# Kernel tuning notes

Hardware: AMD Instinct MI355X
Metric: run time of the kernel (lower is better)

## Reference

```python
import jax, jax.numpy as jnp
import numpy as np

N_TV_ITER = 20      # fixed Chambolle iteration count (skimage early-stops via eps; fixed for jit)
TV_WEIGHT = 0.1


def _div(p):
    # negative adjoint of forward-difference gradient (skimage convention)
    d = -(p[0] + p[1])
    d = d.at[1:, :].add(p[0, :-1, :])
    d = d.at[:, 1:].add(p[1, :, :-1])
    return d


def tv_chambolle_2d(image):
    """skimage.restoration.denoise_tv_chambolle on a single 2D image, weight=0.1."""
    tau = 0.25  # 1 / (2 * ndim)

    def step(p, _):
        out = image + _div(p)
        gy = jnp.zeros_like(out).at[:-1, :].set(out[1:, :] - out[:-1, :])
        gx = jnp.zeros_like(out).at[:, :-1].set(out[:, 1:] - out[:, :-1])
        norm = jnp.sqrt(gy * gy + gx * gx)
        g = jnp.stack([gy, gx])
        p = (p - tau * g) / (1.0 + (tau / TV_WEIGHT) * norm)
        return p, None

    p0 = jnp.zeros((2,) + image.shape, image.dtype)
    p, _ = jax.lax.scan(step, p0, None, length=N_TV_ITER)
    return image + _div(p)


def tv_denoise(img):  # [B,C,H,W], vmapped over B*C (replaces the CPU python loop)
    B, C, H, W = img.shape
    out = jax.vmap(tv_chambolle_2d)(img.reshape(B * C, H, W))
    return out.reshape(B, C, H, W)


def conv(x, w, stride=1, groups=1):
    pad = w.shape[2] // 2  # 'same'-style padding for odd kernels, 0 for 1x1
    return jax.lax.conv_general_dilated(
        x, w, (stride, stride), [(pad, pad), (pad, pad)],
        dimension_numbers=('NCHW', 'OIHW', 'NCHW'),
        feature_group_count=groups)


def haar_ll(x):
    # one level of pywt wavedec2('haar') LL band: 0.5 * sum over each 2x2 block
    return 0.5 * (x[..., ::2, ::2] + x[..., ::2, 1::2] + x[..., 1::2, ::2] + x[..., 1::2, 1::2])


def backbone(x, stem_w, dw_pw):
    # stride-32, 1280-channel EfficientNet-B0-style feature extractor
    x = jax.nn.silu(conv(x, stem_w, stride=2))
    for dw, pw in dw_pw:
        x = jax.nn.silu(conv(x, dw, stride=2, groups=dw.shape[0]))
        x = jax.nn.silu(conv(x, pw))
    return x


def setup_inputs() -> dict:
    key = jax.random.key(0)
    ks = jax.random.split(key, 16)
    B, H, W = 4, 512, 512

    def w(k, o, i, kh, kw):
        return jax.random.normal(k, (o, i, kh, kw), jnp.float32) * (1.0 / np.sqrt(i * kh * kw))

    return {
        "img": jax.random.normal(ks[0], (B, 1, H, W), jnp.float32),
        "stem_w": w(ks[1], 32, 1, 3, 3),
        "dw1_w": w(ks[2], 32, 1, 3, 3),  "pw1_w": w(ks[3], 64, 32, 1, 1),
        "dw2_w": w(ks[4], 64, 1, 3, 3),  "pw2_w": w(ks[5], 128, 64, 1, 1),
        "dw3_w": w(ks[6], 128, 1, 3, 3), "pw3_w": w(ks[7], 256, 128, 1, 1),
        "dw4_w": w(ks[8], 256, 1, 3, 3), "pw4_w": w(ks[9], 512, 256, 1, 1),
        "head_w": w(ks[10], 1280, 512, 1, 1),
        "proj_w": w(ks[11], 64, 1280, 1, 1),
        "proj_b": jnp.zeros((64,), jnp.float32),
        "final_w": w(ks[12], 1, 64, 1, 1),
        "final_b": jnp.zeros((1,), jnp.float32),
    }


def reference(img, stem_w, dw1_w, pw1_w, dw2_w, pw2_w, dw3_w, pw3_w, dw4_w, pw4_w,
              head_w, proj_w, proj_b, final_w, final_b):
    B, C, H, W = img.shape
    x = tv_denoise(img)                                     # fused TV Chambolle
    x = backbone(x, stem_w, [(dw1_w, pw1_w), (dw2_w, pw2_w), (dw3_w, pw3_w), (dw4_w, pw4_w)])
    x = jax.nn.silu(conv(x, head_w))                        # [B,1280,H/32,W/32]
    x = conv(x, proj_w) + proj_b[None, :, None, None]       # [B,64,H/32,W/32]
    x = jax.image.resize(x, (B, 64, H, W), method='bilinear')  # align_corners=False semantics
    ll = haar_ll(haar_ll(x))                                # 2-level Haar LL: [B,64,H/4,W/4]
    out = conv(ll, final_w) + final_b[None, :, None, None]  # [B,1,H/4,W/4]
    return out
```

## Files before the change

### kernel.cpp

```cpp
#include <hip/hip_runtime.h>
#include <math.h>

constexpr int BATCH = 4;
constexpr int IMG_H = 512, IMG_W = 512;
constexpr int IMG_HW = IMG_H * IMG_W;
constexpr int PSTR = BATCH * IMG_HW;

constexpr size_t O_PA   = 0;
constexpr size_t O_PB   = O_PA + 2 * (size_t)PSTR;
constexpr size_t O_DEN  = O_PB + 2 * (size_t)PSTR;
constexpr size_t O_A1   = O_DEN + (size_t)PSTR;
constexpr size_t O_A2   = O_A1 + 8388608;
constexpr size_t O_WT1  = O_A2 + 2097152;
constexpr size_t O_WT2  = O_WT1 + 32 * 64;
constexpr size_t O_WT3  = O_WT2 + 64 * 128;
constexpr size_t O_WT4  = O_WT3 + 128 * 256;
constexpr size_t O_WTH  = O_WT4 + 256 * 512;
constexpr size_t O_WCOMB= O_WTH + 512 * 1280;
constexpr size_t O_BCOMB= O_WCOMB + 1280;
constexpr size_t O_S    = O_BCOMB + 4;
constexpr size_t WS_FLOATS = O_S + 1024;

__device__ __forceinline__ float fast_rcp(float x) { return __builtin_amdgcn_rcpf(x); }
__device__ __forceinline__ float fast_sqrt(float x) { return __builtin_amdgcn_sqrtf(x); }
__device__ __forceinline__ float silu_f(float x) {
    float e = __builtin_amdgcn_exp2f(-1.44269504088896f * x);
    return x * fast_rcp(1.0f + e);
}
__device__ __forceinline__ int clampi(int v, int lo, int hi) {
    return v < lo ? lo : (v > hi ? hi : v);
}

template <int NST, bool FIRST, bool LAST>
__global__ __launch_bounds__(512, 8) void tv_reg(const float* __restrict__ img,
                                                 const float* __restrict__ pin,
                                                 float* __restrict__ pout,
                                                 const float* __restrict__ pw1,
                                                 const float* __restrict__ pw2,
                                                 const float* __restrict__ pw3,
                                                 const float* __restrict__ pw4,
                                                 const float* __restrict__ headw,
                                                 const float* __restrict__ projw,
                                                 const float* __restrict__ projb,
                                                 const float* __restrict__ finalw,
                                                 float* __restrict__ ws) {
    constexpr int ROWS = 6, NW = 8, HL = 10, TC = 44, TR = 28;
    constexpr int TVY = 19;
    __shared__ float bndP[2][512], bndO[2][512];

    if constexpr (FIRST) {
        if (blockIdx.y >= TVY) {
            __shared__ float tt[32][33];
            const int tid = threadIdx.x;
            const int pid = ((blockIdx.y - TVY) * 4 + blockIdx.z) * 12 + blockIdx.x;
            for (int t = pid; t < 814; t += 96) {
                const float* src = nullptr; float* dst = nullptr;
                int C = 0, R = 0, tr = 0, tc = 0;
                if (t < 640) {
                    src = headw; dst = ws + O_WTH; R = 1280; C = 512; tr = t >> 4; tc = t & 15;
                } else if (t < 768) {
                    int e = t - 640; src = pw4; dst = ws + O_WT4; R = 512; C = 256; tr = e >> 3; tc = e & 7;
                } else if (t < 800) {
                    int e = t - 768; src = pw3; dst = ws + O_WT3; R = 256; C = 128; tr = e >> 2; tc = e & 3;
                } else if (t < 808) {
                    int e = t - 800; src = pw2; dst = ws + O_WT2; R = 128; C = 64; tr = e >> 1; tc = e & 1;
                } else if (t < 810) {
                    int e = t - 808; src = pw1; dst = ws + O_WT1; R = 64; C = 32; tr = e; tc = 0;
                }
                const int tx = tid & 31, ty = tid >> 5;
                __syncthreads();
                if (src) {
#pragma unroll
                    for (int j = 0; j < 2; ++j)
                        tt[ty + j * 16][tx] =
                            src[(size_t)(tr * 32 + ty + j * 16) * C + tc * 32 + tx];
                }
                __syncthreads();
                if (src) {
#pragma unroll
                    for (int j = 0; j < 2; ++j)
                        dst[(size_t)(tc * 32 + ty + j * 16) * R + tr * 32 + tx] =
                            tt[tx][ty + j * 16];
                } else if (t < 813) {
                    int k = (t - 810) * 512 + tid;
                    if (k < 1280) {
                        float a = 0.0f;
                        for (int ch = 0; ch < 64; ++ch)
                            a = fmaf(finalw[ch], projw[ch * 1280 + k], a);
                        ws[O_WCOMB + k] = a;
                    }
                } else {
                    if (tid == 0) {
                        float a = 0.0f;
                        for (int ch = 0; ch < 64; ++ch) a = fmaf(finalw[ch], projb[ch], a);
                        ws[O_BCOMB] = a;
                    }
                }
            }
            return;
        }
    }

    const int tid = threadIdx.x;
    const int lane = tid & 63, w = tid >> 6;
    const int b = blockIdx.z;
    const int r0 = blockIdx.y * TR, c0 = blockIdx.x * TC;
    const int gj = c0 - HL + lane;
    const int gjc = clampi(gj, 0, 511);
    const int gib = r0 - HL + w * ROWS;
    const float* I = img + b * IMG_HW;
    const bool interior = (r0 - HL >= 1) && (r0 + NW * ROWS - HL <= 511) &&
                          (c0 - HL >= 1) && (c0 + 64 - HL <= 511);

    float rim[ROWS], rp0[ROWS], rp1[ROWS], ro[ROWS];
#pragma unroll
    for (int k = 0; k < ROWS; ++k) {
        int gi = clampi(gib + k, 0, 511);
        rim[k] = I[(gi << 9) + gjc];
    }
    if (!FIRST) {
        const float* P0 = pin + b * IMG_HW;
        const float* P1 = pin + PSTR + b * IMG_HW;
#pragma unroll
        for (int k = 0; k < ROWS; ++k) {
            int gi = clampi(gib + k, 0, 511);
            rp0[k] = P0[(gi << 9) + gjc];
            rp1[k] = P1[(gi << 9) + gjc];
        }
    }
    const bool gjpos = (gj > 0), gjlt = (gj < 511);

    int s0 = 0;
    if (FIRST) {
        bndO[0][tid] = rim[0];
        __syncthreads();
        float odn = (w < NW - 1) ? bndO[0][tid + 64] : 0.0f;
        if (interior) {
#pragma unroll
            for (int k = 0; k < ROWS; ++k) {
                float oR = __shfl_down(rim[k], 1);
                float od = (k < ROWS - 1) ? rim[k + 1] : odn;
                float gy = od - rim[k];
                float gx = oR - rim[k];
                float inv = fast_rcp(fmaf(2.5f, fast_sqrt(fmaf(gy, gy, gx * gx)), 1.0f));
                rp0[k] = -0.25f * gy * inv;
                rp1[k] = -0.25f * gx * inv;
            }
        } else {
#pragma unroll
            for (int k = 0; k < ROWS; ++k) {
                float oR = __shfl_down(rim[k], 1);
                float od = (k < ROWS - 1) ? rim[k + 1] : odn;
                int gi = gib + k;
                float gy = (gi < 511) ? od - rim[k] : 0.0f;
                float gx = gjlt ? oR - rim[k] : 0.0f;
                float inv = fast_rcp(fmaf(2.5f, fast_sqrt(fmaf(gy, gy, gx * gx)), 1.0f));
                rp0[k] = -0.25f * gy * inv;
                rp1[k] = -0.25f * gx * inv;
            }
        }
        s0 = 1;
    }

    for (int s = s0; s < NST; ++s) {
        const int par = s & 1;
        float p1l0 = __shfl_up(rp1[0], 1);
        float partO = rim[0] - rp0[0] - rp1[0];
        if (interior) partO += p1l0;
        else if (gjpos) partO += p1l0;
        bndP[par][tid] = rp0[ROWS - 1];
        bndO[par][tid] = partO;
        __syncthreads();
        float pup0 = (w > 0) ? bndP[par][tid - 64] : 0.0f;
        float odn = (w < NW - 1) ? bndO[par][tid + 64] + rp0[ROWS - 1] : 0.0f;
        if (interior) {
            ro[0] = partO + pup0;
#pragma unroll
            for (int k = 1; k < ROWS; ++k) {
                float p1l = __shfl_up(rp1[k], 1);
                ro[k] = rim[k] - rp0[k] - rp1[k] + rp0[k - 1] + p1l;
            }
#pragma unroll
            for (int k = 0; k < ROWS; ++k) {
                float oR = __shfl_down(ro[k], 1);
                float od = (k < ROWS - 1) ? ro[k + 1] : odn;
                float gy = od - ro[k];
                float gx = oR - ro[k];
                float inv = fast_rcp(fmaf(2.5f, fast_sqrt(fmaf(gy, gy, gx * gx)), 1.0f));
                rp0[k] = (rp0[k] - 0.25f * gy) * inv;
                rp1[k] = (rp1[k] - 0.25f * gx) * inv;
            }
        } else {
            ro[0] = partO + ((gib > 0) ? pup0 : 0.0f);
#pragma unroll
            for (int k = 1; k < ROWS; ++k) {
                float p1l = __shfl_up(rp1[k], 1);
                float o = rim[k] - rp0[k] - rp1[k];
                if (gib + k > 0) o += rp0[k - 1];
                if (gjpos) o += p1l;
                ro[k] = o;
            }
#pragma unroll
            for (int k = 0; k < ROWS; ++k) {
                float oR = __shfl_down(ro[k], 1);
                float od = (k < ROWS - 1) ? ro[k + 1] : odn;
                int gi = gib + k;
                float gy = (gi < 511) ? od - ro[k] : 0.0f;
                float gx = gjlt ? oR - ro[k] : 0.0f;
                float inv = fast_rcp(fmaf(2.5f, fast_sqrt(fmaf(gy, gy, gx * gx)), 1.0f));
                rp0[k] = (rp0[k] - 0.25f * gy) * inv;
                rp1[k] = (rp1[k] - 0.25f * gx) * inv;
            }
        }
    }

    const bool cst = (lane >= HL && lane < HL + TC && gj < 512);
    if (LAST) {
        constexpr int epar = NST & 1;
        bndP[epar][tid] = rp0[ROWS - 1];
        __syncthreads();
        float pup0 = (w > 0) ? bndP[epar][tid - 64] : 0.0f;
        float* D = pout + b * IMG_HW;
#pragma unroll
        for (int k = 0; k < ROWS; ++k) {
            float p1l = __shfl_up(rp1[k], 1);
            int gi = gib + k;
            int rk = w * ROWS + k;
            float o = rim[k] - rp0[k] - rp1[k];
            float pup = (k > 0) ? rp0[k - 1] : pup0;
            if (gi > 0) o += pup;
            if (gjpos) o += p1l;
            if (rk >= HL && rk < HL + TR && cst && gi < 512) D[(gi << 9) + gj] = o;
        }
    } else {
        float* Q0 = pout + b * IMG_HW;
        float* Q1 = pout + PSTR + b * IMG_HW;
#pragma unroll
        for (int k = 0; k < ROWS; ++k) {
            int rk = w * ROWS + k;
            int gi = gib + k;
            if (rk >= HL && rk < HL + TR && cst && gi < 512) {
                Q0[(gi << 9) + gj] = rp0[k];
                Q1[(gi << 9) + gj] = rp1[k];
            }
        }
    }
}

__global__ __launch_bounds__(256) void stem_dw1_pw1(const float* __restrict__ den,
                                                    const float* __restrict__ stemw,
                                                    const float* __restrict__ dw1w,
                                                    const float* __restrict__ pw1T,
                                                    float* __restrict__ out) {
    __shared__ float sDen[35 * 36];
    __shared__ float sStem[8 * 323];
    __shared__ float sDw[32 * 64];
    __shared__ float sW[576];
    __shared__ __align__(16) float sWp[2048];
    const int tid = threadIdx.x;
    const int b = blockIdx.z;
    const int r0 = blockIdx.y * 32, c0 = blockIdx.x * 32;
    const float* D = den + b * IMG_HW;
    for (int e = tid; e < 576; e += 256) sW[e] = (e < 288) ? stemw[e] : dw1w[e - 288];
    for (int e = tid; e < 2048; e += 256) sWp[e] = pw1T[e];
    for (int e = tid; e < 35 * 35; e += 256) {
        int li = e / 35, lj = e % 35;
        int gi = r0 - 3 + li, gjj = c0 - 3 + lj;
        sDen[li * 36 + lj] = (gi >= 0 && gjj >= 0) ? D[(gi << 9) + gjj] : 0.0f;
    }
    __syncthreads();

    for (int g = 0; g < 4; ++g) {
        if (g) __syncthreads();
        for (int e = tid; e < 2312; e += 256) {
            int pos = e >> 3, cl = e & 7;
            int sy = pos / 17, sx = pos % 17;
            int c = 8 * g + cl;
            const float* wc = &sW[c * 9];
            const float* dbase = &sDen[(2 * sy) * 36 + 2 * sx];
            float a = 0.0f;
#pragma unroll
            for (int ky = 0; ky < 3; ++ky)
#pragma unroll
                for (int kx = 0; kx < 3; ++kx)
                    a = fmaf(wc[ky * 3 + kx], dbase[ky * 36 + kx], a);
            sStem[cl * 323 + sy * 19 + sx] = silu_f(a);
        }
        __syncthreads();
        for (int e = tid; e < 512; e += 256) {
            int cl = e >> 6, dy = (e >> 3) & 7, dx = e & 7;
            int c = 8 * g + cl;
            float acc = 0.0f;
#pragma unroll
            for (int ky = 0; ky < 3; ++ky)
#pragma unroll
                for (int kx = 0; kx < 3; ++kx) {
                    int sgy = (r0 >> 1) - 1 + 2 * dy + ky;
                    int sgx = (c0 >> 1) - 1 + 2 * dx + kx;
                    float v = (sgy >= 0 && sgx >= 0)
                        ? sStem[cl * 323 + (2 * dy + ky) * 19 + 2 * dx + kx] : 0.0f;
                    acc = fmaf(sW[288 + c * 9 + ky * 3 + kx], v, acc);
                }
            sDw[c * 64 + (dy << 3) + dx] = silu_f(acc);
        }
    }
    __syncthreads();

    const int px = tid & 63, oc0 = (tid >> 6) * 16;
    float acc[16];
#pragma unroll
    for (int j = 0; j < 16; ++j) acc[j] = 0.0f;
    for (int ic = 0; ic < 32; ++ic) {
        float v = sDw[ic * 64 + px];
        const float* wr = &sWp[ic * 64 + oc0];
#pragma unroll
        for (int q = 0; q < 4; ++q) {
            float4 w4 = *(const float4*)(wr + q * 4);
            acc[q * 4 + 0] = fmaf(v, w4.x, acc[q * 4 + 0]);
            acc[q * 4 + 1] = fmaf(v, w4.y, acc[q * 4 + 1]);
            acc[q * 4 + 2] = fmaf(v, w4.z, acc[q * 4 + 2]);
            acc[q * 4 + 3] = fmaf(v, w4.w, acc[q * 4 + 3]);
        }
    }
    const int gpos = ((r0 >> 2) + (px >> 3)) * 128 + (c0 >> 2) + (px & 7);
    float* ob = out + (size_t)b * 64 * 16384 + (size_t)oc0 * 16384 + gpos;
#pragma unroll
    for (int j = 0; j < 16; ++j) ob[(size_t)j * 16384] = silu_f(acc[j]);
}

template <int C, int HIN>
__global__ __launch_bounds__(256) void dw_kernel(const float* __restrict__ in,
                                                 const float* __restrict__ w,
                                                 float* __restrict__ out) {
    constexpr int HO = HIN / 2;
    int t = blockIdx.x * 256 + threadIdx.x;
    int x = t % HO;
    int y = (t / HO) % HO;
    int c = (t / (HO * HO)) % C;
    int b = t / (HO * HO * C);
    const float* I = in + ((size_t)(b * C + c)) * (HIN * HIN);
    const float* wc = w + c * 9;
    int iy = 2 * y - 1, ix = 2 * x - 1;
    float acc = 0.0f;
#pragma unroll
    for (int ky = 0; ky < 3; ++ky)
#pragma unroll
        for (int kx = 0; kx < 3; ++kx) {
            int yy = iy + ky, xx = ix + kx;
            float vv = (yy >= 0 && xx >= 0) ? I[yy * HIN + xx] : 0.0f;
            acc = fmaf(wc[ky * 3 + kx], vv, acc);
        }
    out[t] = silu_f(acc);
}

template <int C, int HIN>
__global__ __launch_bounds__(256) void dw_reduce2_kernel(const float* __restrict__ part,
                                                         const float* __restrict__ w,
                                                         float* __restrict__ out) {
    constexpr int HO = HIN / 2;
    int t = blockIdx.x * 256 + threadIdx.x;
    int x = t % HO;
    int y = (t / HO) % HO;
    int c = (t / (HO * HO)) % C;
    int b = t / (HO * HO * C);
    const float* Ia = part + ((size_t)(b * C + c)) * (HIN * HIN);
    const float* Ib = Ia + (size_t)BATCH * C * HIN * HIN;
    const float* wc = w + c * 9;
    int iy = 2 * y - 1, ix = 2 * x - 1;
    float acc = 0.0f;
#pragma unroll
    for (int ky = 0; ky < 3; ++ky)
#pragma unroll
        for (int kx = 0; kx < 3; ++kx) {
            int yy = iy + ky, xx = ix + kx;
            float vv = 0.0f;
            if (yy >= 0 && xx >= 0) {
                int o = yy * HIN + xx;
                vv = silu_f(Ia[o] + Ib[o]);
            }
            acc = fmaf(wc[ky * 3 + kx], vv, acc);
        }
    out[t] = silu_f(acc);
}

template <int ICT, int NSIN, int NSPLIT, int OC, bool SILU>
__global__ __launch_bounds__(256) void pw_gemm(const float* __restrict__ in,
                                               const float* __restrict__ wT,
                                               float* __restrict__ out,
                                               int HW) {
    constexpr int KC = 32, TP = 64, TOC = 64, OPT = 4, PPT = 4;
    constexpr int KS = ICT / NSPLIT;
    constexpr int NC = KS / KC;
    constexpr int NOG = TOC / OPT;
    constexpr int PV4 = KC * TP / 4 / 256;
    constexpr int WV4 = KC * TOC / 4 / 256;
    static_assert(KS % KC == 0, "split");
    __shared__ __align__(16) float sPx[2][KC * TP];
    __shared__ __align__(16) float sW[2][KC * TOC];
    const int tid = threadIdx.x;
    const int zb = blockIdx.z;
    const int b = zb / NSPLIT, ks = zb % NSPLIT;
    const int p0 = blockIdx.x * TP;
    const int oc0 = blockIdx.y * TOC;
    const int ocg = tid % NOG, pxg = tid / NOG;
    const size_t instride = (size_t)BATCH * ICT * HW;
    const float* gin0 = in + ((size_t)b * ICT + ks * KS) * HW + p0;
    const float* gw0  = wT + ((size_t)(ks * KS)) * OC + oc0;

    float4 rp[PV4], rw[WV4];
    auto load_chunk = [&](int cc) {
        const float* gin = gin0 + (size_t)cc * KC * HW;
#pragma unroll
        for (int i = 0; i < PV4; ++i) {
            int e = tid + i * 256;
            int row = e / (TP / 4), col = e % (TP / 4);
            const float* base = gin + (size_t)row * HW + col * 4;
            float4 a = *(const float4*)base;
#pragma unroll
            for (int s = 1; s < NSIN; ++s) {
                float4 t4 = *(const float4*)(base + (size_t)s * instride);
                a.x += t4.x; a.y += t4.y; a.z += t4.z; a.w += t4.w;
            }
            if (NSIN > 1) {
                a.x = silu_f(a.x); a.y = silu_f(a.y);
                a.z = silu_f(a.z); a.w = silu_f(a.w);
            }
            rp[i] = a;
        }
        const float* gw = gw0 + (size_t)cc * KC * OC;
#pragma unroll
        for (int i = 0; i < WV4; ++i) {
            int e = tid + i * 256;
            int row = e / (TOC / 4), col = e % (TOC / 4);
            rw[i] = *(const float4*)(gw + (size_t)row * OC + col * 4);
        }
    };
    auto store_chunk = [&](int buf) {
#pragma unroll
        for (int i = 0; i < PV4; ++i) ((float4*)sPx[buf])[tid + i * 256] = rp[i];
#pragma unroll
        for (int i = 0; i < WV4; ++i) ((float4*)sW[buf])[tid + i * 256] = rw[i];
    };

    float acc[OPT][PPT];
#pragma unroll
    for (int o = 0; o < OPT; ++o)
#pragma unroll
        for (int p = 0; p < PPT; ++p) acc[o][p] = 0.0f;

    load_chunk(0);
    store_chunk(0);
    __syncthreads();
    for (int cc = 0; cc < NC; ++cc) {
        if (cc + 1 < NC) load_chunk(cc + 1);
        const int buf = cc & 1;
#pragma unroll 4
        for (int k = 0; k < KC; ++k) {
            float4 pv = *(const float4*)&sPx[buf][k * TP + pxg * PPT];
            float4 wv = *(const float4*)&sW[buf][k * TOC + ocg * OPT];
            float w0 = wv.x, w1 = wv.y, w2 = wv.z, w3 = wv.w;
            acc[0][0] = fmaf(pv.x, w0, acc[0][0]);
            acc[0][1] = fmaf(pv.y, w0, acc[0][1]);
            acc[0][2] = fmaf(pv.z, w0, acc[0][2]);
            acc[0][3] = fmaf(pv.w, w0, acc[0][3]);
            acc[1][0] = fmaf(pv.x, w1, acc[1][0]);
            acc[1][1] = fmaf(pv.y, w1, acc[1][1]);
            acc[1][2] = fmaf(pv.z, w1, acc[1][2]);
            acc[1][3] = fmaf(pv.w, w1, acc[1][3]);
            acc[2][0] = fmaf(pv.x, w2, acc[2][0]);
            acc[2][1] = fmaf(pv.y, w2, acc[2][1]);
            acc[2][2] = fmaf(pv.z, w2, acc[2][2]);
            acc[2][3] = fmaf(pv.w, w2, acc[2][3]);
            acc[3][0] = fmaf(pv.x, w3, acc[3][0]);
            acc[3][1] = fmaf(pv.y, w3, acc[3][1]);
            acc[3][2] = fmaf(pv.z, w3, acc[3][2]);
            acc[3][3] = fmaf(pv.w, w3, acc[3][3]);
        }
        if (cc + 1 < NC) {
            store_chunk((cc + 1) & 1);
            __syncthreads();
        }
    }

    float* ob;
    if (NSPLIT == 1)
        ob = out + ((size_t)(b * OC + oc0 + ocg * OPT)) * HW + p0 + pxg * PPT;
    else
        ob = out + (((size_t)(ks * BATCH + b)) * OC + oc0 + ocg * OPT) * HW + p0 + pxg * PPT;
#pragma unroll
    for (int o = 0; o < OPT; ++o) {
        float4 r;
        r.x = SILU ? silu_f(acc[o][0]) : acc[o][0];
        r.y = SILU ? silu_f(acc[o][1]) : acc[o][1];
        r.z = SILU ? silu_f(acc[o][2]) : acc[o][2];
        r.w = SILU ? silu_f(acc[o][3]) : acc[o][3];
        *(float4*)(ob + (size_t)o * HW) = r;
    }
}

__global__ __launch_bounds__(256) void head_fused(const float* __restrict__ in,
                                                  const float* __restrict__ wT,
                                                  const float* __restrict__ wcomb,
                                                  float* __restrict__ partial) {
    constexpr int ICT = 512, KC = 32, TP = 32, TOC = 64, OC = 1280, HW = 256;
    constexpr int NC = ICT / KC;
    __shared__ __align__(16) float sPx[2][KC * TP];
    __shared__ __align__(16) float sW[2][KC * TOC];
    __shared__ float red[512];
    const int tid = threadIdx.x;
    const int b = blockIdx.z;
    const int p0 = blockIdx.x * TP;
    const int oc0 = blockIdx.y * TOC;
    const int ocg = tid & 15, pxg = tid >> 4;
    const size_t instride = (size_t)BATCH * ICT * HW;
    const float* gin0 = in + (size_t)b * ICT * HW + p0;

    float4 rp, rw[2];
    auto load_chunk = [&](int cc) {
        const float* gin = gin0 + (size_t)cc * KC * HW;
        {
            int row = tid >> 3, col = tid & 7;
            const float* base = gin + (size_t)row * HW + col * 4;
            float4 a = *(const float4*)base;
#pragma unroll
            for (int s = 1; s < 4; ++s) {
                float4 t4 = *(const float4*)(base + (size_t)s * instride);
                a.x += t4.x; a.y += t4.y; a.z += t4.z; a.w += t4.w;
            }
            a.x = silu_f(a.x); a.y = silu_f(a.y);
            a.z = silu_f(a.z); a.w = silu_f(a.w);
            rp = a;
        }
        const float* gw = wT + ((size_t)cc * KC) * OC + oc0;
#pragma unroll
        for (int i = 0; i < 2; ++i) {
            int e = tid + i * 256;
            int row = e >> 4, col = e & 15;
            rw[i] = *(const float4*)(gw + (size_t)row * OC + col * 4);
        }
    };
    auto store_chunk = [&](int buf) {
        ((float4*)sPx[buf])[tid] = rp;
#pragma unroll
        for (int i = 0; i < 2; ++i) ((float4*)sW[buf])[tid + i * 256] = rw[i];
    };

    float acc[4][2];
#pragma unroll
    for (int o = 0; o < 4; ++o) { acc[o][0] = 0.0f; acc[o][1] = 0.0f; }

    load_chunk(0);
    store_chunk(0);
    __syncthreads();
    for (int cc = 0; cc < NC; ++cc) {
        if (cc + 1 < NC) load_chunk(cc + 1);
        const int buf = cc & 1;
#pragma unroll 4
        for (int k = 0; k < KC; ++k) {
            float2 pv = *(const float2*)&sPx[buf][k * TP + pxg * 2];
            float4 wv = *(const float4*)&sW[buf][k * TOC + ocg * 4];
            acc[0][0] = fmaf(pv.x, wv.x, acc[0][0]);
            acc[0][1] = fmaf(pv.y, wv.x, acc[0][1]);
            acc[1][0] = fmaf(pv.x, wv.y, acc[1][0]);
            acc[1][1] = fmaf(pv.y, wv.y, acc[1][1]);
            acc[2][0] = fmaf(pv.x, wv.z, acc[2][0]);
            acc[2][1] = fmaf(pv.y, wv.z, acc[2][1]);
            acc[3][0] = fmaf(pv.x, wv.w, acc[3][0]);
            acc[3][1] = fmaf(pv.y, wv.w, acc[3][1]);
        }
        if (cc + 1 < NC) {
            store_chunk((cc + 1) & 1);
            __syncthreads();
        }
    }

    float4 wc4 = *(const float4*)(wcomb + oc0 + ocg * 4);
#pragma unroll
    for (int p = 0; p < 2; ++p) {
        float v = wc4.x * silu_f(acc[0][p]);
        v = fmaf(wc4.y, silu_f(acc[1][p]), v);
        v = fmaf(wc4.z, silu_f(acc[2][p]), v);
        v = fmaf(wc4.w, silu_f(acc[3][p]), v);
        red[(pxg * 2 + p) * 16 + ocg] = v;
    }
    __syncthreads();
    if (tid < 32) {
        float a = 0.0f;
#pragma unroll
        for (int g = 0; g < 16; ++g) a += red[tid * 16 + g];
        partial[((size_t)blockIdx.y * 4 + b) * 256 + p0 + tid] = a;
    }
}

__global__ __launch_bounds__(256) void resize_haar(const float* __restrict__ partial,
                                                   const float* __restrict__ bcomb,
                                                   const float* __restrict__ finalb,
                                                   float* __restrict__ out) {
    __shared__ float sS[256];
    int t = blockIdx.x * 256 + threadIdx.x;
    int c = t & 127, r = (t >> 7) & 127, b = t >> 14;
    {
        float a = bcomb[0];
        const float* P = partial + (size_t)b * 256 + threadIdx.x;
        for (int y = 0; y < 20; ++y) a += P[(size_t)y * 1024];
        sS[threadIdx.x] = a;
    }
    __syncthreads();
    const float* S = sS;
    float acc = 0.0f;
#pragma unroll
    for (int j = 0; j < 4; ++j) {
        float sy = ((4 * r + j) + 0.5f) * (1.0f / 32.0f) - 0.5f;
        int y0 = (int)floorf(sy);
        float fy = sy - (float)y0;
        int ya = y0 < 0 ? 0 : y0;
        int yb = (y0 + 1) > 15 ? 15 : (y0 + 1);
#pragma unroll
        for (int i = 0; i < 4; ++i) {
            float sx = ((4 * c + i) + 0.5f) * (1.0f / 32.0f) - 0.5f;
            int x0 = (int)floorf(sx);
            float fx = sx - (float)x0;
            int xa = x0 < 0 ? 0 : x0;
            int xb = (x0 + 1) > 15 ? 15 : (x0 + 1);
            float v0 = S[ya * 16 + xa] * (1.0f - fx) + S[ya * 16 + xb] * fx;
            float v1 = S[yb * 16 + xa] * (1.0f - fx) + S[yb * 16 + xb] * fx;
            acc += v0 * (1.0f - fy) + v1 * fy;
        }
    }
    out[t] = 0.25f * acc + finalb[0];
}

extern "C" void kernel_launch(void* const* d_in, const int* in_sizes, int n_in,
                              void* d_out, int out_size, void* d_ws, size_t ws_size,
                              hipStream_t stream) {
    if (ws_size < WS_FLOATS * sizeof(float)) return;

    const float* img    = (const float*)d_in[0];
    const float* stem_w = (const float*)d_in[1];
    const float* dw1_w  = (const float*)d_in[2];
    const float* pw1_w  = (const float*)d_in[3];
    const float* dw2_w  = (const float*)d_in[4];
    const float* pw2_w  = (const float*)d_in[5];
    const float* dw3_w  = (const float*)d_in[6];
    const float* pw3_w  = (const float*)d_in[7];
    const float* dw4_w  = (const float*)d_in[8];
    const float* pw4_w  = (const float*)d_in[9];
    const float* head_w = (const float*)d_in[10];
    const float* proj_w = (const float*)d_in[11];
    const float* proj_b = (const float*)d_in[12];
    const float* final_w= (const float*)d_in[13];
    const float* final_b= (const float*)d_in[14];
    float* ws  = (float*)d_ws;
    float* out = (float*)d_out;

    dim3 tvg1(12, 21, 4), tvg2(12, 19, 4);
    tv_reg<10, true,  false><<<tvg1, 512, 0, stream>>>(
        img, img, ws + O_PA,
        pw1_w, pw2_w, pw3_w, pw4_w, head_w, proj_w, proj_b, final_w, ws);
    tv_reg<10, false, true ><<<tvg2, 512, 0, stream>>>(
        img, ws + O_PA, ws + O_DEN,
        nullptr, nullptr, nullptr, nullptr, nullptr, nullptr, nullptr, nullptr, ws);

    stem_dw1_pw1<<<dim3(16, 16, 4), 256, 0, stream>>>(ws + O_DEN, stem_w, dw1_w,
                                                      ws + O_WT1, ws + O_A1);

    dw_kernel<64, 128><<<4096, 256, 0, stream>>>(ws + O_A1, dw2_w, ws + O_A2);
    pw_gemm<64, 1, 2, 128, false><<<dim3(64, 2, 8), 256, 0, stream>>>(ws + O_A2, ws + O_WT2, ws + O_PA, 4096);

    dw_reduce2_kernel<128, 64><<<2048, 256, 0, stream>>>(ws + O_PA, dw3_w, ws + O_A1);
    pw_gemm<128, 1, 2, 256, false><<<dim3(16, 4, 8), 256, 0, stream>>>(ws + O_A1, ws + O_WT3, ws + O_PA, 1024);

    dw_reduce2_kernel<256, 32><<<1024, 256, 0, stream>>>(ws + O_PA, dw4_w, ws + O_A2);
    pw_gemm<256, 1, 4, 512, false><<<dim3(4, 8, 16), 256, 0, stream>>>(ws + O_A2, ws + O_WT4, ws + O_PA, 256);

    head_fused<<<dim3(8, 20, 4), 256, 0, stream>>>(ws + O_PA, ws + O_WTH, ws + O_WCOMB, ws + O_A1);

    resize_haar<<<256, 256, 0, stream>>>(ws + O_A1, ws + O_BCOMB, final_b, out);
}
```

Measured before the change: 239.3 us.

## Split head presum into its own kernel and enlarge head GEMM register tile

The 4-way split-K partial sum plus SiLU that used to be recomputed inside every head_fused block (once per output-channel tile) now runs once in a separate presum_silu kernel. head_fused now reads the pre-activated input and computes an 8x4 register tile per thread over 128 output channels and 64 pixels. Weights are read straight from global memory rather than staged in LDS, which makes the grid smaller (160 blocks) and halves the partial count that resize_haar reduces. The trade-offs are an extra kernel launch, an extra intermediate round trip through memory, and lower parallelism in the head GEMM.

Measured after the change: 293.8 us. 22.8% more time.

```diff
diff --git a/kernel.cpp b/kernel.cpp
--- a/kernel.cpp
+++ b/kernel.cpp
@@ -498,96 +498,128 @@
     }
 }
 
-__global__ __launch_bounds__(256) void head_fused(const float* __restrict__ in,
+__global__ __launch_bounds__(256) void presum_silu(const float* __restrict__ part,
+                                                   float* __restrict__ xout) {
+    constexpr size_t PS = (size_t)BATCH * 512 * 256;
+    int t = blockIdx.x * 256 + threadIdx.x;
+    const float* p = part + (size_t)t * 4;
+    float4 a = *(const float4*)p;
+    float4 b = *(const float4*)(p + PS);
+    float4 c = *(const float4*)(p + 2 * PS);
+    float4 d = *(const float4*)(p + 3 * PS);
+    a.x += b.x; a.y += b.y; a.z += b.z; a.w += b.w;
+    a.x += c.x; a.y += c.y; a.z += c.z; a.w += c.w;
+    a.x += d.x; a.y += d.y; a.z += d.z; a.w += d.w;
+    a.x = silu_f(a.x); a.y = silu_f(a.y); a.z = silu_f(a.z); a.w = silu_f(a.w);
+    *(float4*)(xout + (size_t)t * 4) = a;
+}
+
+__global__ __launch_bounds__(256) void head_fused(const float* __restrict__ x,
                                                   const float* __restrict__ wT,
                                                   const float* __restrict__ wcomb,
                                                   float* __restrict__ partial) {
-    constexpr int ICT = 512, KC = 32, TP = 32, TOC = 64, OC = 1280, HW = 256;
-    constexpr int NC = ICT / KC;
+    constexpr int KC = 32, TP = 64, OC = 1280, HW = 256, NC = 16;
     __shared__ __align__(16) float sPx[2][KC * TP];
-    __shared__ __align__(16) float sW[2][KC * TOC];
-    __shared__ float red[512];
+    __shared__ float dotred[64 * 16];
     const int tid = threadIdx.x;
     const int b = blockIdx.z;
     const int p0 = blockIdx.x * TP;
-    const int oc0 = blockIdx.y * TOC;
+    const int oc0 = blockIdx.y * 128;
     const int ocg = tid & 15, pxg = tid >> 4;
-    const size_t instride = (size_t)BATCH * ICT * HW;
-    const float* gin0 = in + (size_t)b * ICT * HW + p0;
-
-    float4 rp, rw[2];
-    auto load_chunk = [&](int cc) {
+    const float* gin0 = x + (size_t)b * 512 * HW + p0;
+    const float* gw0 = wT + oc0 + ocg * 8;
+
+    float4 rp[2];
+    auto load_px = [&](int cc) {
         const float* gin = gin0 + (size_t)cc * KC * HW;
-        {
-            int row = tid >> 3, col = tid & 7;
-            const float* base = gin + (size_t)row * HW + col * 4;
-            float4 a = *(const float4*)base;
-#pragma unroll
-            for (int s = 1; s < 4; ++s) {
-                float4 t4 = *(const float4*)(base + (size_t)s * instride);
-                a.x += t4.x; a.y += t4.y; a.z += t4.z; a.w += t4.w;
-            }
-            a.x = silu_f(a.x); a.y = silu_f(a.y);
-            a.z = silu_f(a.z); a.w = silu_f(a.w);
-            rp = a;
-        }
-        const float* gw = wT + ((size_t)cc * KC) * OC + oc0;
 #pragma unroll
         for (int i = 0; i < 2; ++i) {
             int e = tid + i * 256;
             int row = e >> 4, col = e & 15;
-            rw[i] = *(const float4*)(gw + (size_t)row * OC + col * 4);
+            rp[i] = *(const float4*)(gin + (size_t)row * HW + col * 4);
         }
     };
-    auto store_chunk = [&](int buf) {
-        ((float4*)sPx[buf])[tid] = rp;
-#pragma unroll
-        for (int i = 0; i < 2; ++i) ((float4*)sW[buf])[tid + i * 256] = rw[i];
+    auto store_px = [&](int buf) {
+#pragma unroll
+        for (int i = 0; i < 2; ++i) ((float4*)sPx[buf])[tid + i * 256] = rp[i];
     };
 
-    float acc[4][2];
-#pragma unroll
-    for (int o = 0; o < 4; ++o) { acc[o][0] = 0.0f; acc[o][1] = 0.0f; }
-
-    load_chunk(0);
-    store_chunk(0);
+    float acc[8][4];
+#pragma unroll
+    for (int o = 0; o < 8; ++o)
+#pragma unroll
+        for (int p = 0; p < 4; ++p) acc[o][p] = 0.0f;
+
+    load_px(0);
+    store_px(0);
     __syncthreads();
     for (int cc = 0; cc < NC; ++cc) {
-        if (cc + 1 < NC) load_chunk(cc + 1);
-        const int buf = cc & 1;
-#pragma unroll 4
+        if (cc + 1 < NC) load_px(cc + 1);
+        const float* sp = sPx[cc & 1];
+        const float* gw = gw0 + (size_t)cc * KC * OC;
+#pragma unroll 8
         for (int k = 0; k < KC; ++k) {
-            float2 pv = *(const float2*)&sPx[buf][k * TP + pxg * 2];
-            float4 wv = *(const float4*)&sW[buf][k * TOC + ocg * 4];
-            acc[0][0] = fmaf(pv.x, wv.x, acc[0][0]);
-            acc[0][1] = fmaf(pv.y, wv.x, acc[0][1]);
-            acc[1][0] = fmaf(pv.x, wv.y, acc[1][0]);
-            acc[1][1] = fmaf(pv.y, wv.y, acc[1][1]);
-            acc[2][0] = fmaf(pv.x, wv.z, acc[2][0]);
-            acc[2][1] = fmaf(pv.y, wv.z, acc[2][1]);
-            acc[3][0] = fmaf(pv.x, wv.w, acc[3][0]);
-            acc[3][1] = fmaf(pv.y, wv.w, acc[3][1]);
+            float4 w0 = *(const float4*)(gw + (size_t)k * OC);
+            float4 w1 = *(const float4*)(gw + (size_t)k * OC + 4);
+            float4 pv = *(const float4*)&sp[k * TP + pxg * 4];
+            acc[0][0] = fmaf(pv.x, w0.x, acc[0][0]);
+            acc[0][1] = fmaf(pv.y, w0.x, acc[0][1]);
+            acc[0][2] = fmaf(pv.z, w0.x, acc[0][2]);
+            acc[0][3] = fmaf(pv.w, w0.x, acc[0][3]);
+            acc[1][0] = fmaf(pv.x, w0.y, acc[1][0]);
+            acc[1][1] = fmaf(pv.y, w0.y, acc[1][1]);
+            acc[1][2] = fmaf(pv.z, w0.y, acc[1][2]);
+            acc[1][3] = fmaf(pv.w, w0.y, acc[1][3]);
+            acc[2][0] = fmaf(pv.x, w0.z, acc[2][0]);
+            acc[2][1] = fmaf(pv.y, w0.z, acc[2][1]);
+            acc[2][2] = fmaf(pv.z, w0.z, acc[2][2]);
+            acc[2][3] = fmaf(pv.w, w0.z, acc[2][3]);
+            acc[3][0] = fmaf(pv.x, w0.w, acc[3][0]);
+            acc[3][1] = fmaf(pv.y, w0.w, acc[3][1]);
+            acc[3][2] = fmaf(pv.z, w0.w, acc[3][2]);
+            acc[3][3] = fmaf(pv.w, w0.w, acc[3][3]);
+            acc[4][0] = fmaf(pv.x, w1.x, acc[4][0]);
+            acc[4][1] = fmaf(pv.y, w1.x, acc[4][1]);
+            acc[4][2] = fmaf(pv.z, w1.x, acc[4][2]);
+            acc[4][3] = fmaf(pv.w, w1.x, acc[4][3]);
+            acc[5][0] = fmaf(pv.x, w1.y, acc[5][0]);
+            acc[5][1] = fmaf(pv.y, w1.y, acc[5][1]);
+            acc[5][2] = fmaf(pv.z, w1.y, acc[5][2]);
+            acc[5][3] = fmaf(pv.w, w1.y, acc[5][3]);
+            acc[6][0] = fmaf(pv.x, w1.z, acc[6][0]);
+            acc[6][1] = fmaf(pv.y, w1.z, acc[6][1]);
+            acc[6][2] = fmaf(pv.z, w1.z, acc[6][2]);
+            acc[6][3] = fmaf(pv.w, w1.z, acc[6][3]);
+            acc[7][0] = fmaf(pv.x, w1.w, acc[7][0]);
+            acc[7][1] = fmaf(pv.y, w1.w, acc[7][1]);
+            acc[7][2] = fmaf(pv.z, w1.w, acc[7][2]);
+            acc[7][3] = fmaf(pv.w, w1.w, acc[7][3]);
         }
         if (cc + 1 < NC) {
-            store_chunk((cc + 1) & 1);
+            store_px((cc + 1) & 1);
             __syncthreads();
         }
     }
 
-    float4 wc4 = *(const float4*)(wcomb + oc0 + ocg * 4);
-#pragma unroll
-    for (int p = 0; p < 2; ++p) {
-        float v = wc4.x * silu_f(acc[0][p]);
-        v = fmaf(wc4.y, silu_f(acc[1][p]), v);
-        v = fmaf(wc4.z, silu_f(acc[2][p]), v);
-        v = fmaf(wc4.w, silu_f(acc[3][p]), v);
-        red[(pxg * 2 + p) * 16 + ocg] = v;
+    float4 wcA = *(const float4*)(wcomb + oc0 + ocg * 8);
+    float4 wcB = *(const float4*)(wcomb + oc0 + ocg * 8 + 4);
+#pragma unroll
+    for (int p = 0; p < 4; ++p) {
+        float v = wcA.x * silu_f(acc[0][p]);
+        v = fmaf(wcA.y, silu_f(acc[1][p]), v);
+        v = fmaf(wcA.z, silu_f(acc[2][p]), v);
+        v = fmaf(wcA.w, silu_f(acc[3][p]), v);
+        v = fmaf(wcB.x, silu_f(acc[4][p]), v);
+        v = fmaf(wcB.y, silu_f(acc[5][p]), v);
+        v = fmaf(wcB.z, silu_f(acc[6][p]), v);
+        v = fmaf(wcB.w, silu_f(acc[7][p]), v);
+        dotred[(pxg * 4 + p) * 16 + ocg] = v;
     }
     __syncthreads();
-    if (tid < 32) {
+    if (tid < 64) {
         float a = 0.0f;
 #pragma unroll
-        for (int g = 0; g < 16; ++g) a += red[tid * 16 + g];
+        for (int gg = 0; gg < 16; ++gg) a += dotred[tid * 16 + gg];
         partial[((size_t)blockIdx.y * 4 + b) * 256 + p0 + tid] = a;
     }
 }
@@ -602,7 +634,7 @@
     {
         float a = bcomb[0];
         const float* P = partial + (size_t)b * 256 + threadIdx.x;
-        for (int y = 0; y < 20; ++y) a += P[(size_t)y * 1024];
+        for (int y = 0; y < 10; ++y) a += P[(size_t)y * 1024];
         sS[threadIdx.x] = a;
     }
     __syncthreads();
@@ -673,7 +705,9 @@
     dw_reduce2_kernel<256, 32><<<1024, 256, 0, stream>>>(ws + O_PA, dw4_w, ws + O_A2);
     pw_gemm<256, 1, 4, 512, false><<<dim3(4, 8, 16), 256, 0, stream>>>(ws + O_A2, ws + O_WT4, ws + O_PA, 256);
 
-    head_fused<<<dim3(8, 20, 4), 256, 0, stream>>>(ws + O_PA, ws + O_WTH, ws + O_WCOMB, ws + O_A1);
+    presum_silu<<<512, 256, 0, stream>>>(ws + O_PA, ws + O_A2);
+
+    head_fused<<<dim3(4, 10, 4), 256, 0, stream>>>(ws + O_A2, ws + O_WTH, ws + O_WCOMB, ws + O_A1);
 
     resize_haar<<<256, 256, 0, stream>>>(ws + O_A1, ws + O_BCOMB, final_b, out);
 }
```
